# Optimization experiments

Measured on AMD Instinct MI355X. Metric: run time of the kernel, lower is better.

The kernel has to match this reference:

```python
import jax, jax.numpy as jnp
import numpy as np

SHIFT = 7  # shift_size; pad = 3


def _gn(x, w, b, eps=1e-5):
    # GroupNorm(1, C): normalize over (C,H,W) per sample, affine per channel
    m = jnp.mean(x, axis=(1, 2, 3), keepdims=True)
    v = jnp.var(x, axis=(1, 2, 3), keepdims=True)
    return (x - m) * jax.lax.rsqrt(v + eps) * w[None, :, None, None] + b[None, :, None, None]


def _conv1x1(x, w, b):
    return jnp.einsum('bchw,oc->bohw', x, w) + b[None, :, None, None]


def _gelu(x):
    return jax.nn.gelu(x, approximate=False)


def _shift_h(x, size):
    # CUDA kernel semantics: g = c // ceil(C/size); s = -(g - size//2);
    # out[n,c,h,w] = x[n,c,h+s,w] if in-bounds else 0  (dim=2)
    B, C, H, W = x.shape
    pad = size // 2
    group = -(-C // size)  # ceil
    s = pad - (jnp.arange(C) // group)              # [C], values in [-pad, pad]
    xp = jnp.pad(x, ((0, 0), (0, 0), (pad, pad), (0, 0)))
    idx = jnp.arange(H)[None, :] + s[:, None] + pad  # [C,H], in [0, H+2p-1]
    c = jnp.arange(C)[:, None]
    return xp[:, c, idx, :]


def _shift_w(x, size):
    return _shift_h(x.swapaxes(2, 3), size).swapaxes(2, 3)


def _axial_shift(x, c1w, c1b, n1w, n1b, c21w, c21b, c22w, c22b, n2w, n2b, c3w, c3b):
    x = _gelu(_gn(_conv1x1(x, c1w, c1b), n1w, n1b))
    x_lr = _shift_w(x, SHIFT)
    x_td = _shift_h(x, SHIFT)
    x_lr = _gelu(_conv1x1(x_lr, c21w, c21b))
    x_td = _gelu(_conv1x1(x_td, c22w, c22b))
    x = _gn(x_lr + x_td, n2w, n2b)
    return _conv1x1(x, c3w, c3b)


def setup_inputs() -> dict:
    B, C, H, W = 16, 256, 56, 56
    HID = 4 * C
    key = jax.random.key(0)
    ks = jax.random.split(key, 8)
    wscale = 0.05
    inp = {
        'x': jax.random.normal(ks[0], (B, C, H, W), jnp.float32),
        'n1_w': jnp.ones((C,), jnp.float32), 'n1_b': jnp.zeros((C,), jnp.float32),
        'as_c1_w': jax.random.normal(ks[1], (C, C), jnp.float32) * wscale,
        'as_c1_b': jnp.zeros((C,), jnp.float32),
        'as_n1_w': jnp.ones((C,), jnp.float32), 'as_n1_b': jnp.zeros((C,), jnp.float32),
        'as_c21_w': jax.random.normal(ks[2], (C, C), jnp.float32) * wscale,
        'as_c21_b': jnp.zeros((C,), jnp.float32),
        'as_c22_w': jax.random.normal(ks[3], (C, C), jnp.float32) * wscale,
        'as_c22_b': jnp.zeros((C,), jnp.float32),
        'as_n2_w': jnp.ones((C,), jnp.float32), 'as_n2_b': jnp.zeros((C,), jnp.float32),
        'as_c3_w': jax.random.normal(ks[4], (C, C), jnp.float32) * wscale,
        'as_c3_b': jnp.zeros((C,), jnp.float32),
        'n2_w': jnp.ones((C,), jnp.float32), 'n2_b': jnp.zeros((C,), jnp.float32),
        'fc1_w': jax.random.normal(ks[5], (HID, C), jnp.float32) * wscale,
        'fc1_b': jnp.zeros((HID,), jnp.float32),
        'fc2_w': jax.random.normal(ks[6], (C, HID), jnp.float32) * wscale,
        'fc2_b': jnp.zeros((C,), jnp.float32),
    }
    return inp


def reference(x, n1_w, n1_b, as_c1_w, as_c1_b, as_n1_w, as_n1_b,
              as_c21_w, as_c21_b, as_c22_w, as_c22_b, as_n2_w, as_n2_b,
              as_c3_w, as_c3_b, n2_w, n2_b, fc1_w, fc1_b, fc2_w, fc2_b):
    # AxialShiftedBlock: x = x + AxialShift(norm1(x)); x = x + Mlp(norm2(x))
    h = _gn(x, n1_w, n1_b)
    h = _axial_shift(h, as_c1_w, as_c1_b, as_n1_w, as_n1_b,
                     as_c21_w, as_c21_b, as_c22_w, as_c22_b,
                     as_n2_w, as_n2_b, as_c3_w, as_c3_b)
    x = x + h
    h = _gn(x, n2_w, n2_b)
    h = _gelu(_conv1x1(h, fc1_w, fc1_b))
    h = _conv1x1(h, fc2_w, fc2_b)
    return x + h
```

## Files before the change

### kernel.cpp

```cpp
#include <hip/hip_runtime.h>

typedef __attribute__((ext_vector_type(4))) float f32x4;
typedef __attribute__((ext_vector_type(8))) short bf16x8;
typedef __attribute__((ext_vector_type(4))) unsigned short u16x4;
typedef unsigned short u16;

#define HW 3136
#define NSEG 49
#define NELF 802816.0f
#define EPS 1e-5f

__device__ __forceinline__ short f2bf(float f) {
  union { float f; unsigned u; } v; v.f = f;
  unsigned r = (v.u + 0x7FFFu + ((v.u >> 16) & 1u)) >> 16;
  return (short)r;
}
__device__ __forceinline__ float b2f(u16 u) {
  union { unsigned u; float f; } v; v.u = ((unsigned)u) << 16;
  return v.f;
}
__device__ __forceinline__ float fgelu(float x) {
  float x2 = x * x;
  float u = x * (0.7978845608f + 0.0356774081f * x2);
  float e = __expf(-2.0f * u);
  return x * __builtin_amdgcn_rcpf(1.0f + e);
}
__device__ __forceinline__ void gload16(const void* g, void* l) {
  __builtin_amdgcn_global_load_lds(
      (const __attribute__((address_space(1))) void*)(uintptr_t)g,
      (__attribute__((address_space(3))) void*)(unsigned)(uintptr_t)l,
      16, 0, 0);
}

__global__ void wfold_kernel(const float* __restrict__ c1, const float* __restrict__ c21,
                             const float* __restrict__ c22, const float* __restrict__ c3,
                             const float* __restrict__ fc1, const float* __restrict__ fc2,
                             const float* __restrict__ n1w, const float* __restrict__ an2w,
                             const float* __restrict__ n2w, u16* __restrict__ out) {
  int i = (blockIdx.x * 256 + threadIdx.x) * 4;
  const float* src; int off; const float* scale = nullptr;
  if (i < 65536)       { src = c1;  off = 0;       scale = n1w; }
  else if (i < 131072) { src = c21; off = 65536; }
  else if (i < 196608) { src = c22; off = 131072; }
  else if (i < 262144) { src = c3;  off = 196608;  scale = an2w; }
  else if (i < 524288) { src = fc1; off = 262144;  scale = n2w; }
  else                 { src = fc2; off = 524288; }
  int li = i - off;
  float4 v = *(const float4*)(src + li);
  if (scale) {
    float4 g = *(const float4*)(scale + (li & 255));
    v.x *= g.x; v.y *= g.y; v.z *= g.z; v.w *= g.w;
  }
  u16x4 o4; o4[0] = (u16)f2bf(v.x); o4[1] = (u16)f2bf(v.y); o4[2] = (u16)f2bf(v.z); o4[3] = (u16)f2bf(v.w);
  *(u16x4*)(out + i) = o4;
}

__global__ void rowsum_kernel(const float* __restrict__ c1w, const float* __restrict__ c1b,
                              const float* __restrict__ n1w, const float* __restrict__ n1b,
                              const float* __restrict__ c3w, const float* __restrict__ c3b,
                              const float* __restrict__ an2w, const float* __restrict__ an2b,
                              const float* __restrict__ fc1w, const float* __restrict__ fc1b,
                              const float* __restrict__ n2w, const float* __restrict__ n2b,
                              float* __restrict__ sums) {
  int o = blockIdx.x * 256 + threadIdx.x;
  const float *W, *gw, *gb, *cb; float *Sg, *Sb; int row;
  if (o < 256)      { W = c1w;  gw = n1w;  gb = n1b;  cb = c1b;  Sg = sums;        Sb = sums + 256;  row = o; }
  else if (o < 512) { W = c3w;  gw = an2w; gb = an2b; cb = c3b;  Sg = sums + 512;  Sb = sums + 768;  row = o - 256; }
  else              { W = fc1w; gw = n2w;  gb = n2b;  cb = fc1b; Sg = sums + 1024; Sb = sums + 2048; row = o - 512; }
  float sg = 0.f, sb = 0.f;
  for (int c = 0; c < 256; c += 4) {
    float4 w = *(const float4*)(W + (size_t)row * 256 + c);
    float4 g = *(const float4*)(gw + c);
    float4 b = *(const float4*)(gb + c);
    sg += w.x * g.x + w.y * g.y + w.z * g.z + w.w * g.w;
    sb += w.x * b.x + w.y * b.y + w.z * b.z + w.w * b.w;
  }
  Sg[row] = sg; Sb[row] = sb + cb[row];
}

__global__ __launch_bounds__(256) void t0_kernel(const float* __restrict__ x,
                                                 u16* __restrict__ xT, float* __restrict__ st) {
  __shared__ __align__(16) u16 tile[64 * 256];
  const int t = threadIdx.x;
  const int n = blockIdx.x / NSEG;
  const int hw0 = (blockIdx.x % NSEG) * 64;
  const int pix = t & 63;
  float s = 0.f, q = 0.f;
#pragma unroll
  for (int r = 0; r < 16; ++r) {
    int cq = (t >> 6) + (r << 2);
    int c = cq * 4;
    u16x4 o4;
#pragma unroll
    for (int i = 0; i < 4; ++i) {
      float v = x[((size_t)n * 256 + c + i) * HW + hw0 + pix];
      s += v; q += v * v;
      o4[i] = (u16)f2bf(v);
    }
    int u = cq ^ ((pix & 15) << 2);
    *(u16x4*)((char*)tile + pix * 512 + u * 8) = o4;
  }
  __syncthreads();
  {
    const int p2 = t >> 2;
#pragma unroll
    for (int r = 0; r < 8; ++r) {
      int oct = (t & 3) + (r << 2);
      int up = (2 * oct) ^ ((p2 & 15) << 2);
      bf16x8 v = *(const bf16x8*)((char*)tile + p2 * 512 + up * 8);
      *(bf16x8*)&xT[((size_t)n * HW + hw0 + p2) * 256 + oct * 8] = v;
    }
  }
  __syncthreads();
  float* red = (float*)tile;
  red[t] = s; red[256 + t] = q;
  __syncthreads();
  for (int off = 128; off > 0; off >>= 1) {
    if (t < off) { red[t] += red[t + off]; red[256 + t] += red[256 + t + off]; }
    __syncthreads();
  }
  if (t == 0) { atomicAdd(&st[n * 2], red[0]); atomicAdd(&st[n * 2 + 1], red[256]); }
}

__global__ void e2_kernel(const u16* __restrict__ y, u16* __restrict__ tb,
                          const float* __restrict__ gw, const float* __restrict__ gb,
                          const float* __restrict__ stats) {
  const size_t NG = (size_t)16 * HW * 32;
  for (size_t g = (size_t)blockIdx.x * blockDim.x + threadIdx.x; g < NG;
       g += (size_t)gridDim.x * blockDim.x) {
    size_t base = g * 8;
    int n = (int)(base / 802816);
    int c0 = (int)(base & 255);
    float sm = stats[n * 2], sq = stats[n * 2 + 1];
    float mn = sm * (1.0f / NELF);
    float rstd = rsqrtf(sq * (1.0f / NELF) - mn * mn + EPS);
    bf16x8 v = *(const bf16x8*)(y + base);
    bf16x8 o;
#pragma unroll
    for (int j = 0; j < 8; ++j) {
      float sc = rstd * gw[c0 + j];
      float sh = gb[c0 + j] - mn * sc;
      o[j] = f2bf(fgelu(b2f((u16)v[j]) * sc + sh));
    }
    *(bf16x8*)(tb + base) = o;
  }
}

template<int EPI>
__global__ __launch_bounds__(512, 2) void gemmW2(
    const u16* __restrict__ actT, const u16* __restrict__ wt,
    const float* __restrict__ Sg, const float* __restrict__ Sb,
    const float* __restrict__ stats_in, float* __restrict__ stats_out,
    const u16* __restrict__ residCL, u16* __restrict__ outT)
{
  __shared__ __align__(16) u16 lds[79872];
  const int t = threadIdx.x;
  const int lane = t & 63, wave = t >> 6;
  const int fr = lane & 15, fq = lane >> 4;
  const int wo = wave >> 1, wp = wave & 1;
  const int n = blockIdx.x / 14;
  const int hw0 = (blockIdx.x % 14) * 224;
  const size_t nHW = (size_t)n * HW;

  {
    int u0 = t, u1 = t + 512;
    int r0 = u0 >> 2, sg0 = ((u0 & 3) - (r0 >> 1)) & 3;
    int r1 = u1 >> 2, sg1 = ((u1 & 3) - (r1 >> 1)) & 3;
    const u16* w0 = wt + (size_t)r0 * 256 + sg0 * 8;
    const u16* w1 = wt + (size_t)r1 * 256 + sg1 * 8;
#pragma unroll
    for (int k = 0; k < 8; ++k) {
      gload16(w0 + k * 32, &lds[k * 8192 + wave * 512]);
      gload16(w1 + k * 32, &lds[k * 8192 + 4096 + wave * 512]);
    }
  }

  int aU[4];
#pragma unroll
  for (int os = 0; os < 4; ++os) { int row = wo * 64 + os * 16 + fr; aU[os] = (4 * row + ((fq + (row >> 1)) & 3)) * 8; }
  int bO[7];
#pragma unroll
  for (int ps = 0; ps < 7; ++ps) {
    int pix = wp * 112 + ps * 16 + fr;
    bO[ps] = (pix * 4 + (fq ^ (pix & 3))) * 8;
  }

  const u16* srcB0; const u16* srcB1;
  {
    int v0 = wave * 128 + lane, v1 = v0 + 64;
    int p0 = v0 >> 2, j0 = (v0 & 3) ^ (p0 & 3);
    int p1 = v1 >> 2, j1 = (v1 & 3) ^ (p1 & 3);
    srcB0 = actT + (nHW + hw0 + p0) * 256 + j0 * 8;
    srcB1 = actT + (nHW + hw0 + p1) * 256 + j1 * 8;
  }
  auto stageB = [&](int par, int ks) {
    if (wave < 7) {
      gload16(srcB0 + ks * 32, &lds[65536 + par * 7168 + (wave * 128) * 8]);
      gload16(srcB1 + ks * 32, &lds[65536 + par * 7168 + (wave * 128 + 64) * 8]);
    }
  };

  f32x4 acc[4][7];
#pragma unroll
  for (int a = 0; a < 4; ++a)
#pragma unroll
    for (int b = 0; b < 7; ++b) acc[a][b] = (f32x4){0.f, 0.f, 0.f, 0.f};

  stageB(0, 0);
  __syncthreads();

#pragma unroll
  for (int k = 0; k < 8; ++k) {
    if (k < 7) stageB((k + 1) & 1, k + 1);
    bf16x8 afr[4], bfr[7];
#pragma unroll
    for (int os = 0; os < 4; ++os) afr[os] = *(const bf16x8*)&lds[k * 8192 + aU[os]];
#pragma unroll
    for (int ps = 0; ps < 7; ++ps) bfr[ps] = *(const bf16x8*)&lds[65536 + (k & 1) * 7168 + bO[ps]];
#pragma unroll
    for (int os = 0; os < 4; ++os)
#pragma unroll
      for (int ps = 0; ps < 7; ++ps)
        acc[os][ps] = __builtin_amdgcn_mfma_f32_16x16x32_bf16(afr[os], bfr[ps], acc[os][ps], 0, 0, 0);
    __syncthreads();
  }

  char* tl = (char*)lds;
  float sm = stats_in[n * 2], sq = stats_in[n * 2 + 1];
  float mn = sm * (1.0f / NELF);
  float rstd = rsqrtf(sq * (1.0f / NELF) - mn * mn + EPS);
  float mr = mn * rstd;
  float lsum = 0.f, lsq = 0.f;
#pragma unroll
  for (int os = 0; os < 4; ++os) {
    const int ob = wo * 64 + os * 16 + fq * 4;
    float4 g4 = *(const float4*)&Sg[ob];
    float4 s4 = *(const float4*)&Sb[ob];
    float be[4] = {s4.x - mr * g4.x, s4.y - mr * g4.y, s4.z - mr * g4.z, s4.w - mr * g4.w};
#pragma unroll
    for (int ps = 0; ps < 7; ++ps) {
      const int pix = wp * 112 + ps * 16 + fr;
      u16x4 rv = {0, 0, 0, 0};
      if (EPI == 1) rv = *(const u16x4*)&residCL[(nHW + hw0 + pix) * 256 + ob];
      u16x4 pk;
#pragma unroll
      for (int j = 0; j < 4; ++j) {
        float v = fmaf(acc[os][ps][j], rstd, be[j]);
        if (EPI == 1) v += b2f(rv[j]);
        lsum += v; lsq += v * v;
        pk[j] = (u16)f2bf(v);
      }
      const int qd = wo * 16 + os * 4 + fq;
      const int uq = qd ^ ((pix & 15) << 2);
      *(u16x4*)(tl + pix * 512 + uq * 8) = pk;
    }
  }
  __syncthreads();
#pragma unroll
  for (int r = 0; r < 14; ++r) {
    int idx = t + r * 512;
    int pix = idx >> 5, oct = idx & 31;
    int up = (2 * oct) ^ ((pix & 15) << 2);
    bf16x8 v = *(const bf16x8*)(tl + pix * 512 + up * 8);
    *(bf16x8*)&outT[(nHW + hw0 + pix) * 256 + oct * 8] = v;
  }
  __syncthreads();
  float* red = (float*)lds;
  red[t] = lsum; red[512 + t] = lsq;
  __syncthreads();
  for (int off = 256; off > 0; off >>= 1) {
    if (t < off) { red[t] += red[t + off]; red[512 + t] += red[512 + t + off]; }
    __syncthreads();
  }
  if (t == 0) { atomicAdd(&stats_out[n * 2], red[0]); atomicAdd(&stats_out[n * 2 + 1], red[512]); }
}

__global__ __launch_bounds__(512, 2) void gemm_dual4(
    const u16* __restrict__ tT, const u16* __restrict__ w21, const u16* __restrict__ w22,
    const float* __restrict__ b21, const float* __restrict__ b22,
    float* __restrict__ stats_out, u16* __restrict__ zT)
{
  __shared__ __align__(16) u16 lds[47616];
  const int t = threadIdx.x;
  const int lane = t & 63, wave = t >> 6;
  const int fr = lane & 15, fq = lane >> 4;
  const int n = blockIdx.x / 28;
  const int hw0 = (blockIdx.x % 28) * 112;
  const size_t nHW = (size_t)n * HW;

  const int u = (t < 448) ? t : 447;
  const int jl = u / 112, p = u - jl * 112;
  const int pix = hw0 + p;
  const int wc = pix % 56, hc = pix / 56;

  bf16x8 gA0, gA1, gB0, gB1;
  auto gatherIssue = [&](int ks) {
    int c0 = ks * 32 + jl * 8;
    int g0 = c0 / 37;
    int s0 = 3 - g0;
    int pa0 = pix + s0;           pa0 = pa0 < 0 ? 0 : (pa0 > HW - 1 ? HW - 1 : pa0);
    int pa1 = pix + s0 - 1;       pa1 = pa1 < 0 ? 0 : (pa1 > HW - 1 ? HW - 1 : pa1);
    int pb0 = pix + 56 * s0;      pb0 = pb0 < 0 ? 0 : (pb0 > HW - 1 ? HW - 1 : pb0);
    int pb1 = pix + 56 * (s0 - 1); pb1 = pb1 < 0 ? 0 : (pb1 > HW - 1 ? HW - 1 : pb1);
    gA0 = *(const bf16x8*)(tT + (nHW + pa0) * 256 + c0);
    gA1 = *(const bf16x8*)(tT + (nHW + pa1) * 256 + c0);
    gB0 = *(const bf16x8*)(tT + (nHW + pb0) * 256 + c0);
    gB1 = *(const bf16x8*)(tT + (nHW + pb1) * 256 + c0);
  };
  auto gatherWrite = [&](int par, int ks) {
    int c0 = ks * 32 + jl * 8;
    int g0 = c0 / 37;
    int s0 = 3 - g0;
    int js = (g0 + 1) * 37 - c0; if (js > 8) js = 8;
    bool a0 = (unsigned)(wc + s0) < 56u, a1 = (unsigned)(wc + s0 - 1) < 56u;
    bool b0 = (unsigned)(hc + s0) < 56u, b1 = (unsigned)(hc + s0 - 1) < 56u;
    bf16x8 va, vb;
#pragma unroll
    for (int j = 0; j < 8; ++j) {
      bool lo = j < js;
      va[j] = lo ? (a0 ? gA0[j] : (short)0) : (a1 ? gA1[j] : (short)0);
      vb[j] = lo ? (b0 ? gB0[j] : (short)0) : (b1 ? gB1[j] : (short)0);
    }
    if (t < 448) {
      *(bf16x8*)&lds[32768 + par * 3712 + (jl * 116 + p) * 8] = va;
      *(bf16x8*)&lds[40192 + par * 3712 + (jl * 116 + p) * 8] = vb;
    }
  };
  auto stageW = [&](int par, int ks) {
    int u0 = t; int r0 = u0 >> 2, sg0 = ((u0 & 3) - (r0 >> 1)) & 3;
    int u1 = t + 512; int r1 = u1 >> 2, sg1 = ((u1 & 3) - (r1 >> 1)) & 3;
    gload16(w21 + (size_t)r0 * 256 + ks * 32 + sg0 * 8, &lds[par * 8192 + wave * 512]);
    gload16(w21 + (size_t)r1 * 256 + ks * 32 + sg1 * 8, &lds[par * 8192 + 4096 + wave * 512]);
    gload16(w22 + (size_t)r0 * 256 + ks * 32 + sg0 * 8, &lds[16384 + par * 8192 + wave * 512]);
    gload16(w22 + (size_t)r1 * 256 + ks * 32 + sg1 * 8, &lds[16384 + par * 8192 + 4096 + wave * 512]);
  };

  int aU[2], bP[7];
#pragma unroll
  for (int os = 0; os < 2; ++os) { int row = wave * 32 + os * 16 + fr; aU[os] = (4 * row + ((fq + (row >> 1)) & 3)) * 8; }
#pragma unroll
  for (int ps = 0; ps < 7; ++ps) bP[ps] = (fq * 116 + ps * 16 + fr) * 8;

  f32x4 accA[2][7], accB[2][7];
#pragma unroll
  for (int a = 0; a < 2; ++a)
#pragma unroll
    for (int b = 0; b < 7; ++b) { accA[a][b] = (f32x4){0, 0, 0, 0}; accB[a][b] = (f32x4){0, 0, 0, 0}; }

  gatherIssue(0);
  stageW(0, 0);
  gatherWrite(0, 0);
  gatherIssue(1);
  __syncthreads();

#pragma unroll
  for (int k = 0; k < 8; ++k) {
    if (k < 7) stageW((k + 1) & 1, k + 1);
    bf16x8 afA[2], afB[2], bfA[7], bfB[7];
#pragma unroll
    for (int os = 0; os < 2; ++os) {
      afA[os] = *(const bf16x8*)&lds[(k & 1) * 8192 + aU[os]];
      afB[os] = *(const bf16x8*)&lds[16384 + (k & 1) * 8192 + aU[os]];
    }
#pragma unroll
    for (int ps = 0; ps < 7; ++ps) {
      bfA[ps] = *(const bf16x8*)&lds[32768 + (k & 1) * 3712 + bP[ps]];
      bfB[ps] = *(const bf16x8*)&lds[40192 + (k & 1) * 3712 + bP[ps]];
    }
#pragma unroll
    for (int os = 0; os < 2; ++os)
#pragma unroll
      for (int ps = 0; ps < 7; ++ps) {
        accA[os][ps] = __builtin_amdgcn_mfma_f32_16x16x32_bf16(afA[os], bfA[ps], accA[os][ps], 0, 0, 0);
        accB[os][ps] = __builtin_amdgcn_mfma_f32_16x16x32_bf16(afB[os], bfB[ps], accB[os][ps], 0, 0, 0);
      }
    if (k < 7) {
      gatherWrite((k + 1) & 1, k + 1);
      if (k < 6) gatherIssue(k + 2);
    }
    __syncthreads();
  }

  char* tl = (char*)lds;
  float lsum = 0.f, lsq = 0.f;
#pragma unroll
  for (int os = 0; os < 2; ++os) {
    const int ob = wave * 32 + os * 16 + fq * 4;
    float4 a4 = *(const float4*)&b21[ob];
    float4 c4 = *(const float4*)&b22[ob];
    float ba[4] = {a4.x, a4.y, a4.z, a4.w};
    float bb[4] = {c4.x, c4.y, c4.z, c4.w};
#pragma unroll
    for (int ps = 0; ps < 7; ++ps) {
      const int pixL = ps * 16 + fr;
      u16x4 pk;
#pragma unroll
      for (int j = 0; j < 4; ++j) {
        float z = fgelu(accA[os][ps][j] + ba[j]) + fgelu(accB[os][ps][j] + bb[j]);
        lsum += z; lsq += z * z;
        pk[j] = (u16)f2bf(z);
      }
      const int qd = wave * 8 + os * 4 + fq;
      const int uq = qd ^ ((pixL & 15) << 2);
      *(u16x4*)(tl + pixL * 512 + uq * 8) = pk;
    }
  }
  __syncthreads();
#pragma unroll
  for (int r = 0; r < 7; ++r) {
    int idx = t + r * 512;
    int pixL = idx >> 5, oct = idx & 31;
    int up = (2 * oct) ^ ((pixL & 15) << 2);
    bf16x8 v = *(const bf16x8*)(tl + pixL * 512 + up * 8);
    *(bf16x8*)&zT[(nHW + hw0 + pixL) * 256 + oct * 8] = v;
  }
  __syncthreads();
  float* red = (float*)lds;
  red[t] = lsum; red[512 + t] = lsq;
  __syncthreads();
  for (int off = 256; off > 0; off >>= 1) {
    if (t < off) { red[t] += red[t + off]; red[512 + t] += red[512 + t + off]; }
    __syncthreads();
  }
  if (t == 0) { atomicAdd(&stats_out[n * 2], red[0]); atomicAdd(&stats_out[n * 2 + 1], red[512]); }
}

__global__ __launch_bounds__(512, 2) void mlp3(
    const u16* __restrict__ x2T, const u16* __restrict__ wfc1, const u16* __restrict__ wfc2,
    const float* __restrict__ Sg, const float* __restrict__ Sb, const float* __restrict__ bias2,
    const float* __restrict__ stats_in, float* __restrict__ out_f32)
{
  __shared__ __align__(16) u16 lds[58624];
  const int t = threadIdx.x;
  const int lane = t & 63, wave = t >> 6;
  const int fr = lane & 15, fq = lane >> 4;
  const int n = blockIdx.x / 28;
  const int hw0 = (blockIdx.x % 28) * 112;
  const size_t nHW = (size_t)n * HW;
  const int HOFF = 28928;

#pragma unroll
  for (int i = 0; i < 7; ++i) {
    int u = wave * 448 + i * 64 + lane;
    int j = u / 112, p = u - j * 112;
    bf16x8 v = *(const bf16x8*)(x2T + (nHW + hw0 + p) * 256 + j * 8);
    *(bf16x8*)&lds[(j * 113 + p) * 8] = v;
  }

  float sm = stats_in[n * 2], sq = stats_in[n * 2 + 1];
  float mn = sm * (1.0f / NELF);
  float rstd = rsqrtf(sq * (1.0f / NELF) - mn * mn + EPS);
  float mr = mn * rstd;

  const int arow = wave * 32 + fr;
  const u16* w1base = wfc1 + (size_t)arow * 256 + fq * 8;
  const u16* w2base = wfc2 + (size_t)arow * 1024 + fq * 8;

  f32x4 oacc[2][7];
#pragma unroll
  for (int a = 0; a < 2; ++a)
#pragma unroll
    for (int b = 0; b < 7; ++b) oacc[a][b] = (f32x4){0.f, 0.f, 0.f, 0.f};

  __syncthreads();

  for (int c = 0; c < 4; ++c) {
    f32x4 hacc[2][7];
#pragma unroll
    for (int a = 0; a < 2; ++a)
#pragma unroll
      for (int b = 0; b < 7; ++b) hacc[a][b] = (f32x4){0.f, 0.f, 0.f, 0.f};

    const u16* w1c = w1base + (size_t)c * 65536;
#pragma unroll
    for (int kk = 0; kk < 8; ++kk) {
      bf16x8 a0 = *(const bf16x8*)(w1c + kk * 32);
      bf16x8 a1 = *(const bf16x8*)(w1c + 4096 + kk * 32);
      bf16x8 bfr[7];
#pragma unroll
      for (int ps = 0; ps < 7; ++ps)
        bfr[ps] = *(const bf16x8*)&lds[((kk * 4 + fq) * 113 + ps * 16 + fr) * 8];
#pragma unroll
      for (int ps = 0; ps < 7; ++ps) {
        hacc[0][ps] = __builtin_amdgcn_mfma_f32_16x16x32_bf16(a0, bfr[ps], hacc[0][ps], 0, 0, 0);
        hacc[1][ps] = __builtin_amdgcn_mfma_f32_16x16x32_bf16(a1, bfr[ps], hacc[1][ps], 0, 0, 0);
      }
    }

    {
      const int hcb = c * 256;
#pragma unroll
      for (int os = 0; os < 2; ++os) {
        const int hcl = wave * 32 + os * 16 + fq * 4;
        const int hc = hcb + hcl;
        float4 g4 = *(const float4*)&Sg[hc];
        float4 s4 = *(const float4*)&Sb[hc];
        float be[4] = {s4.x - mr * g4.x, s4.y - mr * g4.y, s4.z - mr * g4.z, s4.w - mr * g4.w};
        const int jH = hcl >> 3;
#pragma unroll
        for (int ps = 0; ps < 7; ++ps) {
          const int pixL = ps * 16 + fr;
          u16x4 pk;
#pragma unroll
          for (int j = 0; j < 4; ++j)
            pk[j] = (u16)f2bf(fgelu(fmaf(hacc[os][ps][j], rstd, be[j])));
          *(u16x4*)&lds[HOFF + (jH * 116 + pixL) * 8 + (fq & 1) * 4] = pk;
        }
      }
    }
    __syncthreads();

    const u16* w2c = w2base + c * 256;
#pragma unroll
    for (int kk = 0; kk < 8; ++kk) {
      bf16x8 a0 = *(const bf16x8*)(w2c + kk * 32);
      bf16x8 a1 = *(const bf16x8*)(w2c + 16384 + kk * 32);
      bf16x8 bfr[7];
#pragma unroll
      for (int ps = 0; ps < 7; ++ps)
        bfr[ps] = *(const bf16x8*)&lds[HOFF + ((kk * 4 + fq) * 116 + ps * 16 + fr) * 8];
#pragma unroll
      for (int ps = 0; ps < 7; ++ps) {
        oacc[0][ps] = __builtin_amdgcn_mfma_f32_16x16x32_bf16(a0, bfr[ps], oacc[0][ps], 0, 0, 0);
        oacc[1][ps] = __builtin_amdgcn_mfma_f32_16x16x32_bf16(a1, bfr[ps], oacc[1][ps], 0, 0, 0);
      }
    }
    __syncthreads();
  }

#pragma unroll
  for (int os = 0; os < 2; ++os) {
    const int ob = wave * 32 + os * 16 + fq * 4;
    float4 b4 = *(const float4*)&bias2[ob];
    float bb[4] = {b4.x, b4.y, b4.z, b4.w};
#pragma unroll
    for (int ps = 0; ps < 7; ++ps) {
      const int pixL = ps * 16 + fr;
      u16x4 rv = *(const u16x4*)&lds[((ob >> 3) * 113 + pixL) * 8 + (ob & 4)];
#pragma unroll
      for (int j = 0; j < 4; ++j) {
        float v = oacc[os][ps][j] + bb[j] + b2f(rv[j]);
        out_f32[((size_t)n * 256 + ob + j) * HW + hw0 + pixL] = v;
      }
    }
  }
}

extern "C" void kernel_launch(void* const* d_in, const int* in_sizes, int n_in,
                              void* d_out, int out_size, void* d_ws, size_t ws_size,
                              hipStream_t stream) {
  const float* x     = (const float*)d_in[0];
  const float* n1_w  = (const float*)d_in[1];
  const float* n1_b  = (const float*)d_in[2];
  const float* c1_w  = (const float*)d_in[3];
  const float* c1_b  = (const float*)d_in[4];
  const float* an1_w = (const float*)d_in[5];
  const float* an1_b = (const float*)d_in[6];
  const float* c21_w = (const float*)d_in[7];
  const float* c21_b = (const float*)d_in[8];
  const float* c22_w = (const float*)d_in[9];
  const float* c22_b = (const float*)d_in[10];
  const float* an2_w = (const float*)d_in[11];
  const float* an2_b = (const float*)d_in[12];
  const float* c3_w  = (const float*)d_in[13];
  const float* c3_b  = (const float*)d_in[14];
  const float* n2_w  = (const float*)d_in[15];
  const float* n2_b  = (const float*)d_in[16];
  const float* fc1_w = (const float*)d_in[17];
  const float* fc1_b = (const float*)d_in[18];
  const float* fc2_w = (const float*)d_in[19];
  const float* fc2_b = (const float*)d_in[20];

  char* ws = (char*)d_ws;
  float* stats = (float*)ws;
  float* sums  = (float*)(ws + 1024);
  u16* wbuf = (u16*)(ws + 16384);
  u16* wb_c1g  = wbuf;
  u16* wb_c21  = wbuf + 65536;
  u16* wb_c22  = wbuf + 131072;
  u16* wb_c3g  = wbuf + 196608;
  u16* wb_fc1g = wbuf + 262144;
  u16* wb_fc2  = wbuf + 524288;
  const size_t AB = 25690112;
  char* A0 = ws + 1638400;
  u16* xT  = (u16*)(A0);
  u16* yT  = (u16*)(A0 + AB);
  u16* tT  = (u16*)(A0 + 2 * AB);
  u16* zT  = (u16*)(A0 + 3 * AB);
  u16* x2T = (u16*)(A0 + 4 * AB);
  float* out = (float*)d_out;

  hipMemsetAsync(stats, 0, 512, stream);
  wfold_kernel<<<768, 256, 0, stream>>>(c1_w, c21_w, c22_w, c3_w, fc1_w, fc2_w,
                                        n1_w, an2_w, n2_w, wbuf);
  rowsum_kernel<<<6, 256, 0, stream>>>(c1_w, c1_b, n1_w, n1_b, c3_w, c3_b, an2_w, an2_b,
                                       fc1_w, fc1_b, n2_w, n2_b, sums);
  t0_kernel<<<784, 256, 0, stream>>>(x, xT, stats + 0);
  gemmW2<0><<<224, 512, 0, stream>>>(xT, wb_c1g, sums, sums + 256,
                                     stats + 0, stats + 32, nullptr, yT);
  e2_kernel<<<2048, 256, 0, stream>>>(yT, tT, an1_w, an1_b, stats + 32);
  gemm_dual4<<<448, 512, 0, stream>>>(tT, wb_c21, wb_c22, c21_b, c22_b, stats + 64, zT);
  gemmW2<1><<<224, 512, 0, stream>>>(zT, wb_c3g, sums + 512, sums + 768,
                                     stats + 64, stats + 96, xT, x2T);
  mlp3<<<448, 512, 0, stream>>>(x2T, wb_fc1g, wb_fc2, sums + 1024, sums + 2048,
                                fc2_b, stats + 96, out);
}
```

Baseline: 265.3 us.

## Software-pipeline fused MLP: overlap next fc1 chunk with current fc2 chunk

Restructures the fused MLP kernel's hidden-dimension loop so that the fc1 GEMM for chunk c+1 is interleaved with the fc2 GEMM for chunk c in the same inner loop. Both sets of MFMAs are issued together. The intent is to give the scheduler more independent matrix work and fewer serialized phases per barrier. The cost is a second 56-register accumulator set live at the same time, which raises register pressure under launch_bounds(512,2) and risks spills.

```diff
diff --git a/kernel.cpp b/kernel.cpp
--- a/kernel.cpp
+++ b/kernel.cpp
@@ -425,7 +425,7 @@
   if (t == 0) { atomicAdd(&stats_out[n * 2], red[0]); atomicAdd(&stats_out[n * 2 + 1], red[512]); }
 }
 
-__global__ __launch_bounds__(512, 2) void mlp3(
+__global__ __launch_bounds__(512, 2) void mlp5(
     const u16* __restrict__ x2T, const u16* __restrict__ wfc1, const u16* __restrict__ wfc2,
     const float* __restrict__ Sg, const float* __restrict__ Sb, const float* __restrict__ bias2,
     const float* __restrict__ stats_in, float* __restrict__ out_f32)
@@ -456,22 +456,42 @@
   const u16* w1base = wfc1 + (size_t)arow * 256 + fq * 8;
   const u16* w2base = wfc2 + (size_t)arow * 1024 + fq * 8;
 
-  f32x4 oacc[2][7];
+  f32x4 oacc[2][7], hacc[2][7];
 #pragma unroll
   for (int a = 0; a < 2; ++a)
 #pragma unroll
-    for (int b = 0; b < 7; ++b) oacc[a][b] = (f32x4){0.f, 0.f, 0.f, 0.f};
-
-  __syncthreads();
-
-  for (int c = 0; c < 4; ++c) {
-    f32x4 hacc[2][7];
-#pragma unroll
-    for (int a = 0; a < 2; ++a)
-#pragma unroll
-      for (int b = 0; b < 7; ++b) hacc[a][b] = (f32x4){0.f, 0.f, 0.f, 0.f};
-
-    const u16* w1c = w1base + (size_t)c * 65536;
+    for (int b = 0; b < 7; ++b) { oacc[a][b] = (f32x4){0.f, 0.f, 0.f, 0.f}; }
+
+  auto prodH = [&](int cc) {
+    const int hcb = cc * 256;
+#pragma unroll
+    for (int os = 0; os < 2; ++os) {
+      const int hcl = wave * 32 + os * 16 + fq * 4;
+      const int hc = hcb + hcl;
+      float4 g4 = *(const float4*)&Sg[hc];
+      float4 s4 = *(const float4*)&Sb[hc];
+      float be[4] = {s4.x - mr * g4.x, s4.y - mr * g4.y, s4.z - mr * g4.z, s4.w - mr * g4.w};
+      const int jH = hcl >> 3;
+#pragma unroll
+      for (int ps = 0; ps < 7; ++ps) {
+        const int pixL = ps * 16 + fr;
+        u16x4 pk;
+#pragma unroll
+        for (int j = 0; j < 4; ++j)
+          pk[j] = (u16)f2bf(fgelu(fmaf(hacc[os][ps][j], rstd, be[j])));
+        *(u16x4*)&lds[HOFF + (jH * 116 + pixL) * 8 + (fq & 1) * 4] = pk;
+      }
+    }
+  };
+
+  __syncthreads();
+
+#pragma unroll
+  for (int a = 0; a < 2; ++a)
+#pragma unroll
+    for (int b = 0; b < 7; ++b) hacc[a][b] = (f32x4){0.f, 0.f, 0.f, 0.f};
+  {
+    const u16* w1c = w1base;
 #pragma unroll
     for (int kk = 0; kk < 8; ++kk) {
       bf16x8 a0 = *(const bf16x8*)(w1c + kk * 32);
@@ -486,46 +506,58 @@
         hacc[1][ps] = __builtin_amdgcn_mfma_f32_16x16x32_bf16(a1, bfr[ps], hacc[1][ps], 0, 0, 0);
       }
     }
-
-    {
-      const int hcb = c * 256;
-#pragma unroll
-      for (int os = 0; os < 2; ++os) {
-        const int hcl = wave * 32 + os * 16 + fq * 4;
-        const int hc = hcb + hcl;
-        float4 g4 = *(const float4*)&Sg[hc];
-        float4 s4 = *(const float4*)&Sb[hc];
-        float be[4] = {s4.x - mr * g4.x, s4.y - mr * g4.y, s4.z - mr * g4.z, s4.w - mr * g4.w};
-        const int jH = hcl >> 3;
-#pragma unroll
-        for (int ps = 0; ps < 7; ++ps) {
-          const int pixL = ps * 16 + fr;
-          u16x4 pk;
-#pragma unroll
-          for (int j = 0; j < 4; ++j)
-            pk[j] = (u16)f2bf(fgelu(fmaf(hacc[os][ps][j], rstd, be[j])));
-          *(u16x4*)&lds[HOFF + (jH * 116 + pixL) * 8 + (fq & 1) * 4] = pk;
-        }
-      }
-    }
-    __syncthreads();
-
+  }
+  prodH(0);
+  __syncthreads();
+
+  for (int c = 0; c < 3; ++c) {
     const u16* w2c = w2base + c * 256;
+    const u16* w1n = w1base + (size_t)(c + 1) * 65536;
+#pragma unroll
+    for (int a = 0; a < 2; ++a)
+#pragma unroll
+      for (int b = 0; b < 7; ++b) hacc[a][b] = (f32x4){0.f, 0.f, 0.f, 0.f};
 #pragma unroll
     for (int kk = 0; kk < 8; ++kk) {
       bf16x8 a0 = *(const bf16x8*)(w2c + kk * 32);
       bf16x8 a1 = *(const bf16x8*)(w2c + 16384 + kk * 32);
-      bf16x8 bfr[7];
+      bf16x8 c0 = *(const bf16x8*)(w1n + kk * 32);
+      bf16x8 c1 = *(const bf16x8*)(w1n + 4096 + kk * 32);
+      bf16x8 bh[7], bb[7];
+#pragma unroll
+      for (int ps = 0; ps < 7; ++ps) {
+        bh[ps] = *(const bf16x8*)&lds[HOFF + ((kk * 4 + fq) * 116 + ps * 16 + fr) * 8];
+        bb[ps] = *(const bf16x8*)&lds[((kk * 4 + fq) * 113 + ps * 16 + fr) * 8];
+      }
+#pragma unroll
+      for (int ps = 0; ps < 7; ++ps) {
+        oacc[0][ps] = __builtin_amdgcn_mfma_f32_16x16x32_bf16(a0, bh[ps], oacc[0][ps], 0, 0, 0);
+        oacc[1][ps] = __builtin_amdgcn_mfma_f32_16x16x32_bf16(a1, bh[ps], oacc[1][ps], 0, 0, 0);
+        hacc[0][ps] = __builtin_amdgcn_mfma_f32_16x16x32_bf16(c0, bb[ps], hacc[0][ps], 0, 0, 0);
+        hacc[1][ps] = __builtin_amdgcn_mfma_f32_16x16x32_bf16(c1, bb[ps], hacc[1][ps], 0, 0, 0);
+      }
+    }
+    __syncthreads();
+    prodH(c + 1);
+    __syncthreads();
+  }
+
+  {
+    const u16* w2c = w2base + 3 * 256;
+#pragma unroll
+    for (int kk = 0; kk < 8; ++kk) {
+      bf16x8 a0 = *(const bf16x8*)(w2c + kk * 32);
+      bf16x8 a1 = *(const bf16x8*)(w2c + 16384 + kk * 32);
+      bf16x8 bh[7];
 #pragma unroll
       for (int ps = 0; ps < 7; ++ps)
-        bfr[ps] = *(const bf16x8*)&lds[HOFF + ((kk * 4 + fq) * 116 + ps * 16 + fr) * 8];
+        bh[ps] = *(const bf16x8*)&lds[HOFF + ((kk * 4 + fq) * 116 + ps * 16 + fr) * 8];
 #pragma unroll
       for (int ps = 0; ps < 7; ++ps) {
-        oacc[0][ps] = __builtin_amdgcn_mfma_f32_16x16x32_bf16(a0, bfr[ps], oacc[0][ps], 0, 0, 0);
-        oacc[1][ps] = __builtin_amdgcn_mfma_f32_16x16x32_bf16(a1, bfr[ps], oacc[1][ps], 0, 0, 0);
-      }
-    }
-    __syncthreads();
+        oacc[0][ps] = __builtin_amdgcn_mfma_f32_16x16x32_bf16(a0, bh[ps], oacc[0][ps], 0, 0, 0);
+        oacc[1][ps] = __builtin_amdgcn_mfma_f32_16x16x32_bf16(a1, bh[ps], oacc[1][ps], 0, 0, 0);
+      }
+    }
   }
 
 #pragma unroll
@@ -602,6 +634,6 @@
   gemm_dual4<<<448, 512, 0, stream>>>(tT, wb_c21, wb_c22, c21_b, c22_b, stats + 64, zT);
   gemmW2<1><<<224, 512, 0, stream>>>(zT, wb_c3g, sums + 512, sums + 768,
                                      stats + 64, stats + 96, xT, x2T);
-  mlp3<<<448, 512, 0, stream>>>(x2T, wb_fc1g, wb_fc2, sums + 1024, sums + 2048,
+  mlp5<<<448, 512, 0, stream>>>(x2T, wb_fc1g, wb_fc2, sums + 1024, sums + 2048,
                                 fc2_b, stats + 96, out);
 }
```

Result: no change. 266.1 us (+0.3%).
